# Kernel tuning notes

Measured on AMD Instinct MI355X. Metric: run time of the kernel, lower is better.

The kernel has to match this reference:

```python
import math
import jax, jax.numpy as jnp
import numpy as np

EMBED_DIM = 512
NUM_HEADS = 8
PROJ_DIM = EMBED_DIM // NUM_HEADS
ATTN_WINDOW = 5
HALF_WINDOW = (ATTN_WINDOW - 1) // 2  # 2
ATTN_PARAM = 1.0
ATTN_DISPLACEMENT = 1
# per-head positions: ['center','left','right','center'] repeated to 8 heads (synst repeats short lists)
HEAD_SHIFTS = np.array([0, -ATTN_DISPLACEMENT, ATTN_DISPLACEMENT, 0] * 2, dtype=np.int32)


def _xavier(key, shape):
    fan_in, fan_out = shape[1], shape[0]
    bound = math.sqrt(6.0 / (fan_in + fan_out))
    return jax.random.uniform(key, shape, jnp.float32, -bound, bound)


def setup_inputs() -> dict:
    key = jax.random.key(0)
    k1, k2, k3, k4, k5 = jax.random.split(key, 5)
    B, S, E = 8, 4096, EMBED_DIM
    return {
        "values": jax.random.normal(k1, (B, S, E), jnp.float32),
        "keys": jax.random.normal(k2, (B, S, E), jnp.float32),
        "queries": jax.random.normal(k3, (B, S, E), jnp.float32),
        "input_weights": _xavier(k4, (E, E)),        # value projection (attn_weights=1, non-learned type)
        "out_proj_w": _xavier(k5, (E, E)),           # output_projection.weight (bias=False)
    }


def reference(values, keys, queries, input_weights, out_proj_w):
    # keys/queries are unused by the hard-coded 'normal' attention path (no QK^T)
    B, S, E = values.shape
    H, Dh, hw, W = NUM_HEADS, PROJ_DIM, HALF_WINDOW, ATTN_WINDOW

    # value projection + head split: [B,S,E] -> [B,H,S,Dh]
    v = values @ input_weights.T
    v = v.reshape(B, S, H, Dh).transpose(0, 2, 1, 3)

    # fixed Gaussian filter over relative distances [-hw, hw] (unnormalized pdf, as in the source)
    dist = jnp.arange(-hw, hw + 1, dtype=jnp.float32)
    filt = (1.0 / (ATTN_PARAM * math.sqrt(2.0 * math.pi))) * jnp.exp(-0.5 * (dist / ATTN_PARAM) ** 2)  # [W]

    shifts = jnp.asarray(HEAD_SHIFTS)            # [H] per-head center displacement
    P = hw + int(np.max(np.abs(HEAD_SHIFTS)))    # pad so all gathers are in range
    vp = jnp.pad(v, ((0, 0), (0, 0), (P, P), (0, 0)))  # [B,H,S+2P,Dh]

    h_ar = jnp.arange(H)[:, None]                # [H,1]
    pos = jnp.arange(S)[None, :]                 # [1,S]
    out = jnp.zeros_like(v)
    for j in range(W):                           # tiny fixed window loop (W=5)
        idx = pos + P + shifts[:, None] + (j - hw)   # [H,S]
        out = out + filt[j] * vp[:, h_ar, idx, :]    # [B,H,S,Dh]

    out = out.transpose(0, 2, 1, 3).reshape(B, S, E)
    return out @ out_proj_w.T
```

## Files before the change

kernel.cpp:

```cpp
#include <hip/hip_runtime.h>
#include <hip/hip_bf16.h>
#include <stdint.h>

typedef __bf16 bf16;
typedef __bf16 bf16x8 __attribute__((ext_vector_type(8)));
typedef float  f32x4  __attribute__((ext_vector_type(4)));

#define BM 128
#define BN 128
#define BK 64
#define E  512
#define SB 4112
#define M1 (8 * SB)
#define M2 32768

__device__ __forceinline__ void gl_lds_16(const bf16* g, bf16* l) {
    __builtin_amdgcn_global_load_lds(
        (__attribute__((address_space(1))) void*)g,
        (__attribute__((address_space(3))) void*)l,
        16, 0, 0);
}

__global__ __launch_bounds__(256)
void gemm_bt_bf16(const bf16* __restrict__ A, const bf16* __restrict__ Bm,
                  bf16* __restrict__ C, int M, int N, int K)
{
    __shared__ bf16 As[BM * BK];
    __shared__ bf16 Bs[BN * BK];

    const int tid  = threadIdx.x;
    const int id   = blockIdx.x;
    const int bm   = id >> 2;
    const int bn   = id & 3;
    const int wave = tid >> 6;
    const int lane = tid & 63;
    const int wm   = wave >> 1;
    const int wn   = wave & 1;

    const int srow = tid >> 3;
    const int scol = (((tid & 7) ^ (srow & 7)) << 3);
    const size_t a_off = (size_t)(bm * BM + srow) * K + scol;
    const size_t b_off = (size_t)(bn * BN + srow) * K + scol;
    const int    l_off = tid * 8;

    f32x4 acc[4][4] = {};
    const int fr = lane & 15;
    const int q  = lane >> 4;

    for (int k0 = 0; k0 < K; k0 += BK) {
#pragma unroll
        for (int c = 0; c < 4; ++c) {
            gl_lds_16(A  + a_off + (size_t)(c * 32) * K + k0, As + c * 2048 + l_off);
            gl_lds_16(Bm + b_off + (size_t)(c * 32) * K + k0, Bs + c * 2048 + l_off);
        }
        __syncthreads();

#pragma unroll
        for (int t = 0; t < 2; ++t) {
            bf16x8 af[4], bfr[4];
#pragma unroll
            for (int i = 0; i < 4; ++i) {
                const int Ra = wm * 64 + i * 16 + fr;
                const int Rb = wn * 64 + i * 16 + fr;
                const int c  = t * 4 + q;
                af[i]  = *(const bf16x8*)(As + Ra * BK + ((c ^ (Ra & 7)) << 3));
                bfr[i] = *(const bf16x8*)(Bs + Rb * BK + ((c ^ (Rb & 7)) << 3));
            }
#pragma unroll
            for (int i = 0; i < 4; ++i)
#pragma unroll
                for (int j = 0; j < 4; ++j)
                    acc[i][j] = __builtin_amdgcn_mfma_f32_16x16x32_bf16(af[i], bfr[j], acc[i][j], 0, 0, 0);
        }
        __syncthreads();
    }

    const int crow = (lane >> 4) << 2;
    const int ccol = lane & 15;
    const int row0 = bm * BM + wm * 64 + crow;
    const int col0 = bn * BN + wn * 64 + ccol;
#pragma unroll
    for (int i = 0; i < 4; ++i)
#pragma unroll
        for (int j = 0; j < 4; ++j)
#pragma unroll
            for (int r = 0; r < 4; ++r)
                C[(size_t)(row0 + i * 16 + r) * N + (col0 + j * 16)] = (bf16)acc[i][j][r];
}

__global__ __launch_bounds__(256)
void gemm2_gather(const bf16* __restrict__ P, const bf16* __restrict__ Bm,
                  float* __restrict__ C)
{
    __shared__ bf16 As[BM * BK];
    __shared__ bf16 Bs[BN * BK];

    const int tid  = threadIdx.x;
    const int id   = blockIdx.x;
    const int bm   = id >> 2;
    const int bn   = id & 3;
    const int wave = tid >> 6;
    const int lane = tid & 63;
    const int wm   = wave >> 1;
    const int wn   = wave & 1;

    const int srow = tid >> 3;
    const int scol = (((tid & 7) ^ (srow & 7)) << 3);
    const size_t b_off = (size_t)(bn * BN + srow) * E + scol;
    const int    l_off = tid * 8;

    f32x4 acc[4][4] = {};
    const int fr = lane & 15;
    const int q  = lane >> 4;

    for (int k0 = 0; k0 < E; k0 += BK) {
        const int h3 = (k0 >> 6) & 3;
        const int sh = (h3 == 1) ? -1 : (h3 == 2) ? 1 : 0;
#pragma unroll
        for (int c = 0; c < 4; ++c) {
            const int m = bm * BM + c * 32 + srow;
            const int prow = (m >> 12) * SB + (m & 4095) + 1 + sh;
            gl_lds_16(P  + (size_t)prow * E + k0 + scol,          As + c * 2048 + l_off);
            gl_lds_16(Bm + b_off + (size_t)(c * 32) * E + k0,     Bs + c * 2048 + l_off);
        }
        __syncthreads();

#pragma unroll
        for (int t = 0; t < 2; ++t) {
            bf16x8 af[4], bfr[4];
#pragma unroll
            for (int i = 0; i < 4; ++i) {
                const int Ra = wm * 64 + i * 16 + fr;
                const int Rb = wn * 64 + i * 16 + fr;
                const int c  = t * 4 + q;
                af[i]  = *(const bf16x8*)(As + Ra * BK + ((c ^ (Ra & 7)) << 3));
                bfr[i] = *(const bf16x8*)(Bs + Rb * BK + ((c ^ (Rb & 7)) << 3));
            }
#pragma unroll
            for (int i = 0; i < 4; ++i)
#pragma unroll
                for (int j = 0; j < 4; ++j)
                    acc[i][j] = __builtin_amdgcn_mfma_f32_16x16x32_bf16(af[i], bfr[j], acc[i][j], 0, 0, 0);
        }
        __syncthreads();
    }

    const int crow = (lane >> 4) << 2;
    const int ccol = lane & 15;
    const int row0 = bm * BM + wm * 64 + crow;
    const int col0 = bn * BN + wn * 64 + ccol;
#pragma unroll
    for (int i = 0; i < 4; ++i)
#pragma unroll
        for (int j = 0; j < 4; ++j)
#pragma unroll
            for (int r = 0; r < 4; ++r)
                C[(size_t)(row0 + i * 16 + r) * E + (col0 + j * 16)] = acc[i][j][r];
}

__global__ __launch_bounds__(256)
void prep(const float* __restrict__ vals, const float* __restrict__ w_in,
          const float* __restrict__ w_out, bf16* __restrict__ vg,
          bf16* __restrict__ win_b, bf16* __restrict__ wout_b)
{
    const int tid = threadIdx.x;
    const int blk = blockIdx.x;

    if (blk < 256) {
        const int i = blk * 256 + tid;
        const int half = (E * E) / 8;
        const float* src = (i < half) ? w_in : w_out;
        bf16* dst        = (i < half) ? win_b : wout_b;
        const int k = (i < half) ? i : i - half;
        const f32x4* p = (const f32x4*)src + 2 * (size_t)k;
        f32x4 a = p[0], bq = p[1];
        bf16x8 o;
        o[0] = (bf16)a[0];  o[1] = (bf16)a[1];  o[2] = (bf16)a[2];  o[3] = (bf16)a[3];
        o[4] = (bf16)bq[0]; o[5] = (bf16)bq[1]; o[6] = (bf16)bq[2]; o[7] = (bf16)bq[3];
        *((bf16x8*)dst + k) = o;
        return;
    }

    const int e8   = tid & 63;
    const int gidx = (blk - 256) * 4 + (tid >> 6);
    const int m0   = gidx << 3;
    const int b    = m0 / SB;
    const int r0   = m0 - b * SB;

    const float filt[5] = {0.05399096651318806f, 0.24197072451914337f,
                           0.3989422804014327f,
                           0.24197072451914337f, 0.05399096651318806f};

    float acc[8][8];
#pragma unroll
    for (int t = 0; t < 8; ++t)
#pragma unroll
        for (int d = 0; d < 8; ++d) acc[t][d] = 0.f;

    const float* bbase = vals + (size_t)b * 4096 * E + e8 * 8;
#pragma unroll
    for (int u = 0; u < 12; ++u) {
        const int sp = r0 - 3 + u;
        if (sp >= 0 && sp < 4096) {
            const f32x4* p = (const f32x4*)(bbase + (size_t)sp * E);
            const f32x4 x0 = p[0], x1 = p[1];
            const float x[8] = {x0[0], x0[1], x0[2], x0[3],
                                x1[0], x1[1], x1[2], x1[3]};
#pragma unroll
            for (int t = 0; t < 8; ++t) {
                const int j = u - t;
                if (j >= 0 && j < 5) {
                    const float w = filt[j];
#pragma unroll
                    for (int d = 0; d < 8; ++d) acc[t][d] += w * x[d];
                }
            }
        }
    }
#pragma unroll
    for (int t = 0; t < 8; ++t) {
        bf16x8 o;
#pragma unroll
        for (int d = 0; d < 8; ++d) o[d] = (bf16)acc[t][d];
        *((bf16x8*)vg + (size_t)(m0 + t) * 64 + e8) = o;
    }
}

extern "C" void kernel_launch(void* const* d_in, const int* in_sizes, int n_in,
                              void* d_out, int out_size, void* d_ws, size_t ws_size,
                              hipStream_t stream)
{
    const float* values = (const float*)d_in[0];
    const float* w_in   = (const float*)d_in[3];
    const float* w_out  = (const float*)d_in[4];
    float* out = (float*)d_out;

    bf16* win_b  = (bf16*)d_ws;
    bf16* wout_b = win_b + E * E;
    bf16* vg     = wout_b + E * E;
    bf16* Pbuf   = vg + (size_t)M1 * E;

    prep<<<256 + M1 / 32, 256, 0, stream>>>(values, w_in, w_out, vg, win_b, wout_b);

    gemm_bt_bf16<<<(M1 / BM) * 4, 256, 0, stream>>>(vg, win_b, Pbuf, M1, E, E);
    gemm2_gather<<<(M2 / BM) * 4, 256, 0, stream>>>(Pbuf, wout_b, out);
}
```

Baseline: 244.4 us.

## Pipeline both GEMMs with a 3-stage LDS ring and BK=32 MFMA-native layout

```diff
diff --git a/kernel.cpp b/kernel.cpp
--- a/kernel.cpp
+++ b/kernel.cpp
@@ -6,13 +6,11 @@
 typedef __bf16 bf16x8 __attribute__((ext_vector_type(8)));
 typedef float  f32x4  __attribute__((ext_vector_type(4)));
 
-#define BM 128
-#define BN 128
-#define BK 64
 #define E  512
 #define SB 4112
 #define M1 (8 * SB)
 #define M2 32768
+#define NT 16
 
 __device__ __forceinline__ void gl_lds_16(const bf16* g, bf16* l) {
     __builtin_amdgcn_global_load_lds(
@@ -21,12 +19,12 @@
         16, 0, 0);
 }
 
-__global__ __launch_bounds__(256)
+
+__global__ __launch_bounds__(256, 3)
 void gemm_bt_bf16(const bf16* __restrict__ A, const bf16* __restrict__ Bm,
                   bf16* __restrict__ C, int M, int N, int K)
 {
-    __shared__ bf16 As[BM * BK];
-    __shared__ bf16 Bs[BN * BK];
+    __shared__ bf16 ring[3][8192];
 
     const int tid  = threadIdx.x;
     const int id   = blockIdx.x;
@@ -37,48 +35,56 @@
     const int wm   = wave >> 1;
     const int wn   = wave & 1;
 
-    const int srow = tid >> 3;
-    const int scol = (((tid & 7) ^ (srow & 7)) << 3);
-    const size_t a_off = (size_t)(bm * BM + srow) * K + scol;
-    const size_t b_off = (size_t)(bn * BN + srow) * K + scol;
-    const int    l_off = tid * 8;
+    const int gr0  = ((tid >> 6) << 4) + (tid & 15);
+    const int gcol = ((tid >> 4) & 3) << 3;
+    const size_t a_base = (size_t)(bm * 128 + gr0) * K + gcol;
+    const size_t b_base = (size_t)(bn * 128 + gr0) * K + gcol;
 
     f32x4 acc[4][4] = {};
     const int fr = lane & 15;
     const int q  = lane >> 4;
 
-    for (int k0 = 0; k0 < K; k0 += BK) {
-#pragma unroll
-        for (int c = 0; c < 4; ++c) {
-            gl_lds_16(A  + a_off + (size_t)(c * 32) * K + k0, As + c * 2048 + l_off);
-            gl_lds_16(Bm + b_off + (size_t)(c * 32) * K + k0, Bs + c * 2048 + l_off);
+    auto stage = [&](int t, int p) {
+        const size_t gk = (size_t)t << 5;
+        bf16* buf = ring[p];
+        gl_lds_16(A  + a_base + gk,                  buf + tid * 8);
+        gl_lds_16(A  + a_base + (size_t)64 * K + gk, buf + (256 + tid) * 8);
+        gl_lds_16(Bm + b_base + gk,                  buf + 4096 + tid * 8);
+        gl_lds_16(Bm + b_base + (size_t)64 * K + gk, buf + 4096 + (256 + tid) * 8);
+    };
+
+    stage(0, 0);
+    stage(1, 1);
+    __asm__ volatile("s_waitcnt vmcnt(4)" ::: "memory");
+    __asm__ volatile("s_barrier" ::: "memory");
+
+#pragma unroll
+    for (int t = 0; t < NT; ++t) {
+        if (t + 2 < NT) stage(t + 2, (t + 2) % 3);
+
+        const bf16* Ab = ring[t % 3];
+        const bf16* Bb = ring[t % 3] + 4096;
+        bf16x8 af[4], bfv[4];
+#pragma unroll
+        for (int i = 0; i < 4; ++i) {
+            af[i]  = *(const bf16x8*)(Ab + (((wm * 4 + i) * 64) + q * 16 + fr) * 8);
+            bfv[i] = *(const bf16x8*)(Bb + (((wn * 4 + i) * 64) + q * 16 + fr) * 8);
         }
-        __syncthreads();
-
-#pragma unroll
-        for (int t = 0; t < 2; ++t) {
-            bf16x8 af[4], bfr[4];
-#pragma unroll
-            for (int i = 0; i < 4; ++i) {
-                const int Ra = wm * 64 + i * 16 + fr;
-                const int Rb = wn * 64 + i * 16 + fr;
-                const int c  = t * 4 + q;
-                af[i]  = *(const bf16x8*)(As + Ra * BK + ((c ^ (Ra & 7)) << 3));
-                bfr[i] = *(const bf16x8*)(Bs + Rb * BK + ((c ^ (Rb & 7)) << 3));
-            }
-#pragma unroll
-            for (int i = 0; i < 4; ++i)
-#pragma unroll
-                for (int j = 0; j < 4; ++j)
-                    acc[i][j] = __builtin_amdgcn_mfma_f32_16x16x32_bf16(af[i], bfr[j], acc[i][j], 0, 0, 0);
-        }
-        __syncthreads();
+#pragma unroll
+        for (int i = 0; i < 4; ++i)
+#pragma unroll
+            for (int j = 0; j < 4; ++j)
+                acc[i][j] = __builtin_amdgcn_mfma_f32_16x16x32_bf16(af[i], bfv[j], acc[i][j], 0, 0, 0);
+
+        if (t < NT - 2)      __asm__ volatile("s_waitcnt vmcnt(4)" ::: "memory");
+        else if (t == NT - 2) __asm__ volatile("s_waitcnt vmcnt(0)" ::: "memory");
+        if (t < NT - 1)      __asm__ volatile("s_barrier" ::: "memory");
     }
 
     const int crow = (lane >> 4) << 2;
     const int ccol = lane & 15;
-    const int row0 = bm * BM + wm * 64 + crow;
-    const int col0 = bn * BN + wn * 64 + ccol;
+    const int row0 = bm * 128 + wm * 64 + crow;
+    const int col0 = bn * 128 + wn * 64 + ccol;
 #pragma unroll
     for (int i = 0; i < 4; ++i)
 #pragma unroll
@@ -88,12 +94,11 @@
                 C[(size_t)(row0 + i * 16 + r) * N + (col0 + j * 16)] = (bf16)acc[i][j][r];
 }
 
-__global__ __launch_bounds__(256)
+__global__ __launch_bounds__(256, 3)
 void gemm2_gather(const bf16* __restrict__ P, const bf16* __restrict__ Bm,
                   float* __restrict__ C)
 {
-    __shared__ bf16 As[BM * BK];
-    __shared__ bf16 Bs[BN * BK];
+    __shared__ bf16 ring[3][8192];
 
     const int tid  = threadIdx.x;
     const int id   = blockIdx.x;
@@ -104,51 +109,61 @@
     const int wm   = wave >> 1;
     const int wn   = wave & 1;
 
-    const int srow = tid >> 3;
-    const int scol = (((tid & 7) ^ (srow & 7)) << 3);
-    const size_t b_off = (size_t)(bn * BN + srow) * E + scol;
-    const int    l_off = tid * 8;
+    const int gr0  = ((tid >> 6) << 4) + (tid & 15);
+    const int gcol = ((tid >> 4) & 3) << 3;
+    const int m0   = bm * 128 + gr0;
+    const int pr0  = (m0 >> 12) * SB + (m0 & 4095) + 1;
+    const int m1   = m0 + 64;
+    const int pr1  = (m1 >> 12) * SB + (m1 & 4095) + 1;
+    const size_t b_base = (size_t)(bn * 128 + gr0) * E + gcol;
 
     f32x4 acc[4][4] = {};
     const int fr = lane & 15;
     const int q  = lane >> 4;
 
-    for (int k0 = 0; k0 < E; k0 += BK) {
-        const int h3 = (k0 >> 6) & 3;
+    auto stage = [&](int t, int p) {
+        const size_t gk = (size_t)t << 5;
+        const int h3 = (t >> 1) & 3;
         const int sh = (h3 == 1) ? -1 : (h3 == 2) ? 1 : 0;
-#pragma unroll
-        for (int c = 0; c < 4; ++c) {
-            const int m = bm * BM + c * 32 + srow;
-            const int prow = (m >> 12) * SB + (m & 4095) + 1 + sh;
-            gl_lds_16(P  + (size_t)prow * E + k0 + scol,          As + c * 2048 + l_off);
-            gl_lds_16(Bm + b_off + (size_t)(c * 32) * E + k0,     Bs + c * 2048 + l_off);
+        bf16* buf = ring[p];
+        gl_lds_16(P  + (size_t)(pr0 + sh) * E + gcol + gk,   buf + tid * 8);
+        gl_lds_16(P  + (size_t)(pr1 + sh) * E + gcol + gk,   buf + (256 + tid) * 8);
+        gl_lds_16(Bm + b_base + gk,                          buf + 4096 + tid * 8);
+        gl_lds_16(Bm + b_base + (size_t)64 * E + gk,         buf + 4096 + (256 + tid) * 8);
+    };
+
+    stage(0, 0);
+    stage(1, 1);
+    __asm__ volatile("s_waitcnt vmcnt(4)" ::: "memory");
+    __asm__ volatile("s_barrier" ::: "memory");
+
+#pragma unroll
+    for (int t = 0; t < NT; ++t) {
+        if (t + 2 < NT) stage(t + 2, (t + 2) % 3);
+
+        const bf16* Ab = ring[t % 3];
+        const bf16* Bb = ring[t % 3] + 4096;
+        bf16x8 af[4], bfv[4];
+#pragma unroll
+        for (int i = 0; i < 4; ++i) {
+            af[i]  = *(const bf16x8*)(Ab + (((wm * 4 + i) * 64) + q * 16 + fr) * 8);
+            bfv[i] = *(const bf16x8*)(Bb + (((wn * 4 + i) * 64) + q * 16 + fr) * 8);
         }
-        __syncthreads();
-
-#pragma unroll
-        for (int t = 0; t < 2; ++t) {
-            bf16x8 af[4], bfr[4];
-#pragma unroll
-            for (int i = 0; i < 4; ++i) {
-                const int Ra = wm * 64 + i * 16 + fr;
-                const int Rb = wn * 64 + i * 16 + fr;
-                const int c  = t * 4 + q;
-                af[i]  = *(const bf16x8*)(As + Ra * BK + ((c ^ (Ra & 7)) << 3));
-                bfr[i] = *(const bf16x8*)(Bs + Rb * BK + ((c ^ (Rb & 7)) << 3));
-            }
-#pragma unroll
-            for (int i = 0; i < 4; ++i)
-#pragma unroll
-                for (int j = 0; j < 4; ++j)
-                    acc[i][j] = __builtin_amdgcn_mfma_f32_16x16x32_bf16(af[i], bfr[j], acc[i][j], 0, 0, 0);
-        }
-        __syncthreads();
+#pragma unroll
+        for (int i = 0; i < 4; ++i)
+#pragma unroll
+            for (int j = 0; j < 4; ++j)
+                acc[i][j] = __builtin_amdgcn_mfma_f32_16x16x32_bf16(af[i], bfv[j], acc[i][j], 0, 0, 0);
+
+        if (t < NT - 2)      __asm__ volatile("s_waitcnt vmcnt(4)" ::: "memory");
+        else if (t == NT - 2) __asm__ volatile("s_waitcnt vmcnt(0)" ::: "memory");
+        if (t < NT - 1)      __asm__ volatile("s_barrier" ::: "memory");
     }
 
     const int crow = (lane >> 4) << 2;
     const int ccol = lane & 15;
-    const int row0 = bm * BM + wm * 64 + crow;
-    const int col0 = bn * BN + wn * 64 + ccol;
+    const int row0 = bm * 128 + wm * 64 + crow;
+    const int col0 = bn * 128 + wn * 64 + ccol;
 #pragma unroll
     for (int i = 0; i < 4; ++i)
 #pragma unroll
@@ -242,6 +257,6 @@
 
     prep<<<256 + M1 / 32, 256, 0, stream>>>(values, w_in, w_out, vg, win_b, wout_b);
 
-    gemm_bt_bf16<<<(M1 / BM) * 4, 256, 0, stream>>>(vg, win_b, Pbuf, M1, E, E);
-    gemm2_gather<<<(M2 / BM) * 4, 256, 0, stream>>>(Pbuf, wout_b, out);
-}
+    gemm_bt_bf16<<<(M1 / 128) * 4, 256, 0, stream>>>(vg, win_b, Pbuf, M1, E, E);
+    gemm2_gather<<<(M2 / 128) * 4, 256, 0, stream>>>(Pbuf, wout_b, out);
+}
```

Result: slower. 264.7 us (+8.3%).

## Halve GEMM N-tile to 64 and remap blocks for XCD-aware scheduling

Applied to the files above, without the earlier changes.

```diff
diff --git a/kernel.cpp b/kernel.cpp
--- a/kernel.cpp
+++ b/kernel.cpp
@@ -7,7 +7,7 @@
 typedef float  f32x4  __attribute__((ext_vector_type(4)));
 
 #define BM 128
-#define BN 128
+#define BN 64
 #define BK 64
 #define E  512
 #define SB 4112
@@ -21,6 +21,7 @@
         16, 0, 0);
 }
 
+
 __global__ __launch_bounds__(256)
 void gemm_bt_bf16(const bf16* __restrict__ A, const bf16* __restrict__ Bm,
                   bf16* __restrict__ C, int M, int N, int K)
@@ -29,9 +30,10 @@
     __shared__ bf16 Bs[BN * BK];
 
     const int tid  = threadIdx.x;
-    const int id   = blockIdx.x;
-    const int bm   = id >> 2;
-    const int bn   = id & 3;
+    const int nq   = gridDim.x >> 3;
+    const int orig = (blockIdx.x & 7) * nq + (blockIdx.x >> 3);
+    const int bm   = orig >> 3;
+    const int bn   = orig & 7;
     const int wave = tid >> 6;
     const int lane = tid & 63;
     const int wm   = wave >> 1;
@@ -43,33 +45,38 @@
     const size_t b_off = (size_t)(bn * BN + srow) * K + scol;
     const int    l_off = tid * 8;
 
-    f32x4 acc[4][4] = {};
+    f32x4 acc[4][2] = {};
     const int fr = lane & 15;
     const int q  = lane >> 4;
 
     for (int k0 = 0; k0 < K; k0 += BK) {
 #pragma unroll
-        for (int c = 0; c < 4; ++c) {
-            gl_lds_16(A  + a_off + (size_t)(c * 32) * K + k0, As + c * 2048 + l_off);
+        for (int c = 0; c < 4; ++c)
+            gl_lds_16(A + a_off + (size_t)(c * 32) * K + k0, As + c * 2048 + l_off);
+#pragma unroll
+        for (int c = 0; c < 2; ++c)
             gl_lds_16(Bm + b_off + (size_t)(c * 32) * K + k0, Bs + c * 2048 + l_off);
-        }
         __syncthreads();
 
 #pragma unroll
         for (int t = 0; t < 2; ++t) {
-            bf16x8 af[4], bfr[4];
+            bf16x8 af[4], bfr[2];
 #pragma unroll
             for (int i = 0; i < 4; ++i) {
                 const int Ra = wm * 64 + i * 16 + fr;
-                const int Rb = wn * 64 + i * 16 + fr;
-                const int c  = t * 4 + q;
-                af[i]  = *(const bf16x8*)(As + Ra * BK + ((c ^ (Ra & 7)) << 3));
-                bfr[i] = *(const bf16x8*)(Bs + Rb * BK + ((c ^ (Rb & 7)) << 3));
+                const int c  = t * 4 + q;
+                af[i] = *(const bf16x8*)(As + Ra * BK + ((c ^ (Ra & 7)) << 3));
+            }
+#pragma unroll
+            for (int j = 0; j < 2; ++j) {
+                const int Rb = wn * 32 + j * 16 + fr;
+                const int c  = t * 4 + q;
+                bfr[j] = *(const bf16x8*)(Bs + Rb * BK + ((c ^ (Rb & 7)) << 3));
             }
 #pragma unroll
             for (int i = 0; i < 4; ++i)
 #pragma unroll
-                for (int j = 0; j < 4; ++j)
+                for (int j = 0; j < 2; ++j)
                     acc[i][j] = __builtin_amdgcn_mfma_f32_16x16x32_bf16(af[i], bfr[j], acc[i][j], 0, 0, 0);
         }
         __syncthreads();
@@ -78,11 +85,11 @@
     const int crow = (lane >> 4) << 2;
     const int ccol = lane & 15;
     const int row0 = bm * BM + wm * 64 + crow;
-    const int col0 = bn * BN + wn * 64 + ccol;
+    const int col0 = bn * BN + wn * 32 + ccol;
 #pragma unroll
     for (int i = 0; i < 4; ++i)
 #pragma unroll
-        for (int j = 0; j < 4; ++j)
+        for (int j = 0; j < 2; ++j)
 #pragma unroll
             for (int r = 0; r < 4; ++r)
                 C[(size_t)(row0 + i * 16 + r) * N + (col0 + j * 16)] = (bf16)acc[i][j][r];
@@ -96,9 +103,10 @@
     __shared__ bf16 Bs[BN * BK];
 
     const int tid  = threadIdx.x;
-    const int id   = blockIdx.x;
-    const int bm   = id >> 2;
-    const int bn   = id & 3;
+    const int nq   = gridDim.x >> 3;
+    const int orig = (blockIdx.x & 7) * nq + (blockIdx.x >> 3);
+    const int bm   = orig >> 3;
+    const int bn   = orig & 7;
     const int wave = tid >> 6;
     const int lane = tid & 63;
     const int wm   = wave >> 1;
@@ -109,7 +117,7 @@
     const size_t b_off = (size_t)(bn * BN + srow) * E + scol;
     const int    l_off = tid * 8;
 
-    f32x4 acc[4][4] = {};
+    f32x4 acc[4][2] = {};
     const int fr = lane & 15;
     const int q  = lane >> 4;
 
@@ -120,26 +128,32 @@
         for (int c = 0; c < 4; ++c) {
             const int m = bm * BM + c * 32 + srow;
             const int prow = (m >> 12) * SB + (m & 4095) + 1 + sh;
-            gl_lds_16(P  + (size_t)prow * E + k0 + scol,          As + c * 2048 + l_off);
-            gl_lds_16(Bm + b_off + (size_t)(c * 32) * E + k0,     Bs + c * 2048 + l_off);
-        }
+            gl_lds_16(P + (size_t)prow * E + k0 + scol, As + c * 2048 + l_off);
+        }
+#pragma unroll
+        for (int c = 0; c < 2; ++c)
+            gl_lds_16(Bm + b_off + (size_t)(c * 32) * E + k0, Bs + c * 2048 + l_off);
         __syncthreads();
 
 #pragma unroll
         for (int t = 0; t < 2; ++t) {
-            bf16x8 af[4], bfr[4];
+            bf16x8 af[4], bfr[2];
 #pragma unroll
             for (int i = 0; i < 4; ++i) {
                 const int Ra = wm * 64 + i * 16 + fr;
-                const int Rb = wn * 64 + i * 16 + fr;
-                const int c  = t * 4 + q;
-                af[i]  = *(const bf16x8*)(As + Ra * BK + ((c ^ (Ra & 7)) << 3));
-                bfr[i] = *(const bf16x8*)(Bs + Rb * BK + ((c ^ (Rb & 7)) << 3));
+                const int c  = t * 4 + q;
+                af[i] = *(const bf16x8*)(As + Ra * BK + ((c ^ (Ra & 7)) << 3));
+            }
+#pragma unroll
+            for (int j = 0; j < 2; ++j) {
+                const int Rb = wn * 32 + j * 16 + fr;
+                const int c  = t * 4 + q;
+                bfr[j] = *(const bf16x8*)(Bs + Rb * BK + ((c ^ (Rb & 7)) << 3));
             }
 #pragma unroll
             for (int i = 0; i < 4; ++i)
 #pragma unroll
-                for (int j = 0; j < 4; ++j)
+                for (int j = 0; j < 2; ++j)
                     acc[i][j] = __builtin_amdgcn_mfma_f32_16x16x32_bf16(af[i], bfr[j], acc[i][j], 0, 0, 0);
         }
         __syncthreads();
@@ -148,11 +162,11 @@
     const int crow = (lane >> 4) << 2;
     const int ccol = lane & 15;
     const int row0 = bm * BM + wm * 64 + crow;
-    const int col0 = bn * BN + wn * 64 + ccol;
+    const int col0 = bn * BN + wn * 32 + ccol;
 #pragma unroll
     for (int i = 0; i < 4; ++i)
 #pragma unroll
-        for (int j = 0; j < 4; ++j)
+        for (int j = 0; j < 2; ++j)
 #pragma unroll
             for (int r = 0; r < 4; ++r)
                 C[(size_t)(row0 + i * 16 + r) * E + (col0 + j * 16)] = acc[i][j][r];
@@ -242,6 +256,6 @@
 
     prep<<<256 + M1 / 32, 256, 0, stream>>>(values, w_in, w_out, vg, win_b, wout_b);
 
-    gemm_bt_bf16<<<(M1 / BM) * 4, 256, 0, stream>>>(vg, win_b, Pbuf, M1, E, E);
-    gemm2_gather<<<(M2 / BM) * 4, 256, 0, stream>>>(Pbuf, wout_b, out);
-}
+    gemm_bt_bf16<<<(M1 / BM) * 8, 256, 0, stream>>>(vg, win_b, Pbuf, M1, E, E);
+    gemm2_gather<<<(M2 / BM) * 8, 256, 0, stream>>>(Pbuf, wout_b, out);
+}
```

Result: faster. 236.4 us, median of 2 (-3.3%).
